# Kernel optimization log

Hardware: AMD Instinct MI355X
Metric: run time of the kernel (lower is better)

Reference implementation:

```python
import jax, jax.numpy as jnp
import numpy as np

BN_EPS = 1e-5
N_OUT, D_OUT = 64, 128


def setup_inputs() -> dict:
    key = jax.random.key(0)
    k1, k2, k3, k4 = jax.random.split(key, 4)
    B, N_in, D_in, K = 512, 64, 128, 4
    x = jax.random.normal(k1, (B, N_in, D_in), dtype=jnp.float32)
    # block-sparse weights: one (D_in x D_out) block per (output-row, active-input-row) pair
    W = jax.random.normal(k2, (N_OUT, K, D_in, D_OUT), dtype=jnp.float32) * (1.0 / np.sqrt(K * D_in))
    bias = jax.random.normal(k3, (N_OUT, D_OUT), dtype=jnp.float32) * 0.02
    gamma = jnp.ones((N_OUT * D_OUT,), dtype=jnp.float32)
    beta = jnp.zeros((N_OUT * D_OUT,), dtype=jnp.float32)
    idx = jax.random.randint(k4, (N_OUT, K), 0, N_in, dtype=jnp.int32)
    return {"x": x, "W": W, "bias": bias, "gamma": gamma, "beta": beta, "idx": idx}


def reference(x, W, bias, gamma, beta, idx):
    B = x.shape[0]
    # structured-sparse linear: gather active input rows, per-block matmul
    xg = x[:, idx, :]                                   # [B, N_out, K, D_in]
    y = jnp.einsum('bokd,okde->boe', xg, W) + bias      # [B, N_out, D_out]
    # BatchNorm1d (training-mode batch statistics) on flattened features
    yf = y.reshape(B, -1)                               # [B, N_out*D_out]
    mean = jnp.mean(yf, axis=0)
    var = jnp.mean(jnp.square(yf - mean), axis=0)       # biased variance, as in torch BN
    yn = (yf - mean) * jax.lax.rsqrt(var + BN_EPS) * gamma + beta
    # Swish: z * sigmoid(z)
    out = yn * jax.nn.sigmoid(yn)
    return out.reshape(B, N_OUT, D_OUT)
```

## Files before the change

### kernel.cpp

```cpp
#include <hip/hip_runtime.h>


typedef __attribute__((ext_vector_type(8))) __bf16 bf16x8;
typedef __attribute__((ext_vector_type(4))) float  f32x4;

#define FEAT 8192
#define LDA  40

#define PIPE_BARRIER() do { \
    __builtin_amdgcn_sched_barrier(0); \
    asm volatile("s_waitcnt lgkmcnt(0)" ::: "memory"); \
    __builtin_amdgcn_s_barrier(); \
    __builtin_amdgcn_sched_barrier(0); \
} while (0)

__global__ __launch_bounds__(1024, 4)
void fused_encoder(const float* __restrict__ x, const float* __restrict__ W,
                   const float* __restrict__ bias, const float* __restrict__ gamma,
                   const float* __restrict__ beta, const int* __restrict__ idxp,
                   float* __restrict__ out)
{
    __shared__ alignas(16) __bf16 Alds[2][512 * LDA];
    __shared__ alignas(16) __bf16 Blds[2][32 * LDA];
    __shared__ float Sred[16][32];
    __shared__ float Qred[16][32];
    __shared__ float sscale[32];
    __shared__ float sshift[32];

    const int bid = blockIdx.x;
    const int o   = ((bid >> 5) << 3) | (bid & 7);
    const int es  = (bid >> 3) & 3;
    const int e0  = es * 32;

    const int tid  = threadIdx.x;
    const int wave = tid >> 6;
    const int lane = tid & 63;
    const int lam  = lane & 15;
    const int quad = lane >> 4;

    int rsel[4];
#pragma unroll
    for (int k = 0; k < 4; ++k) rsel[k] = idxp[o * 4 + k];

    const f32x4 zero4 = {0.f, 0.f, 0.f, 0.f};
    f32x4 acc[2][2];
#pragma unroll
    for (int mi = 0; mi < 2; ++mi)
#pragma unroll
        for (int ni = 0; ni < 2; ++ni) acc[mi][ni] = zero4;

    const int m_a = tid >> 1;
    const int ca  = (tid & 1) * 16;
    const int e_b = tid & 31;
    const int d_b = tid >> 5;

    f32x4 sA0[4], sA1[4];
    float sB0, sB1;

    auto load_stage = [&](f32x4 (&SA)[4], float& SB, const int kkc) {
        const int kidx  = kkc >> 2;
        const int dbase = (kkc & 3) * 32;
        const float* xa = x + ((m_a * 64 + rsel[kidx]) * 128 + dbase + ca);
#pragma unroll
        for (int v = 0; v < 4; ++v) SA[v] = *(const f32x4*)(xa + v * 4);
        SB = W[(((o * 4 + kidx) * 128) + dbase + d_b) * 128 + e0 + e_b];
    };

    auto store_stage = [&](const f32x4 (&SA)[4], const float SB, const int buf) {
        bf16x8 p0, p1;
#pragma unroll
        for (int j = 0; j < 4; ++j) {
            p0[j]     = (__bf16)SA[0][j];
            p0[j + 4] = (__bf16)SA[1][j];
            p1[j]     = (__bf16)SA[2][j];
            p1[j + 4] = (__bf16)SA[3][j];
        }
        *(bf16x8*)&Alds[buf][m_a * LDA + ca]     = p0;
        *(bf16x8*)&Alds[buf][m_a * LDA + ca + 8] = p1;
        Blds[buf][e_b * LDA + d_b] = (__bf16)SB;
    };

    auto compute = [&](const int buf) {
        bf16x8 af[2], bfr[2];
#pragma unroll
        for (int mi = 0; mi < 2; ++mi)
            af[mi] = *(const bf16x8*)&Alds[buf][(wave * 32 + mi * 16 + lam) * LDA + quad * 8];
#pragma unroll
        for (int ni = 0; ni < 2; ++ni)
            bfr[ni] = *(const bf16x8*)&Blds[buf][(ni * 16 + lam) * LDA + quad * 8];
#pragma unroll
        for (int mi = 0; mi < 2; ++mi)
#pragma unroll
            for (int ni = 0; ni < 2; ++ni)
                acc[mi][ni] = __builtin_amdgcn_mfma_f32_16x16x32_bf16(
                    af[mi], bfr[ni], acc[mi][ni], 0, 0, 0);
    };

    load_stage(sA0, sB0, 0);
    load_stage(sA1, sB1, 1);
    store_stage(sA0, sB0, 0);
    PIPE_BARRIER();

#pragma unroll
    for (int kk = 0; kk < 16; ++kk) {
        if (kk + 2 < 16) {
            if ((kk & 1) == 0) load_stage(sA0, sB0, kk + 2);
            else               load_stage(sA1, sB1, kk + 2);
        }
        __builtin_amdgcn_sched_barrier(0);
        compute(kk & 1);
        if (kk + 1 < 16) {
            if ((kk & 1) == 0) store_stage(sA1, sB1, 1);
            else               store_stage(sA0, sB0, 0);
            PIPE_BARRIER();
        }
    }

    float bvals[2];
#pragma unroll
    for (int ni = 0; ni < 2; ++ni)
        bvals[ni] = bias[o * 128 + e0 + ni * 16 + lam];
#pragma unroll
    for (int mi = 0; mi < 2; ++mi)
#pragma unroll
        for (int ni = 0; ni < 2; ++ni)
#pragma unroll
            for (int rr = 0; rr < 4; ++rr) acc[mi][ni][rr] += bvals[ni];

#pragma unroll
    for (int ni = 0; ni < 2; ++ni) {
        float s = 0.f, q = 0.f;
#pragma unroll
        for (int mi = 0; mi < 2; ++mi)
#pragma unroll
            for (int rr = 0; rr < 4; ++rr) {
                const float v = acc[mi][ni][rr];
                s += v; q += v * v;
            }
        s += __shfl_xor(s, 16); s += __shfl_xor(s, 32);
        q += __shfl_xor(q, 16); q += __shfl_xor(q, 32);
        if (quad == 0) {
            Sred[wave][ni * 16 + lam] = s;
            Qred[wave][ni * 16 + lam] = q;
        }
    }
    __syncthreads();

    if (tid < 32) {
        float s = 0.f, q = 0.f;
#pragma unroll
        for (int w = 0; w < 16; ++w) {
            s += Sred[w][tid];
            q += Qred[w][tid];
        }
        const float mean = s * (1.0f / 512.0f);
        const float var  = q * (1.0f / 512.0f) - mean * mean;
        const float rstd = rsqrtf(var + 1e-5f);
        const float sc   = rstd * gamma[o * 128 + e0 + tid];
        sscale[tid] = sc;
        sshift[tid] = beta[o * 128 + e0 + tid] - mean * sc;
    }
    __syncthreads();

#pragma unroll
    for (int mi = 0; mi < 2; ++mi) {
        const int rowb = wave * 32 + mi * 16 + quad * 4;
#pragma unroll
        for (int ni = 0; ni < 2; ++ni) {
            const int col = ni * 16 + lam;
            const float sc = sscale[col];
            const float sh = sshift[col];
#pragma unroll
            for (int rr = 0; rr < 4; ++rr) {
                const float xn = acc[mi][ni][rr] * sc + sh;
                const float sg = 1.0f / (1.0f + __expf(-xn));
                out[(rowb + rr) * FEAT + o * 128 + e0 + col] = xn * sg;
            }
        }
    }
}

extern "C" void kernel_launch(void* const* d_in, const int* in_sizes, int n_in,
                              void* d_out, int out_size, void* d_ws, size_t ws_size,
                              hipStream_t stream)
{
    const float* x     = (const float*)d_in[0];
    const float* W     = (const float*)d_in[1];
    const float* bias  = (const float*)d_in[2];
    const float* gamma = (const float*)d_in[3];
    const float* beta  = (const float*)d_in[4];
    const int*   idx   = (const int*)d_in[5];
    float* out = (float*)d_out;

    fused_encoder<<<dim3(256), dim3(1024), 0, stream>>>(
        x, W, bias, gamma, beta, idx, out);
}
```

Baseline: 104.0 us.

## Tile blocks over batch and full output width with cooperative grid-sync BN reduction

Each block now covers 128 batch rows and all 128 output columns of one output group, instead of all 512 batch rows and 32 columns. The batch statistics are therefore split across blocks. Per-block partial sums go to workspace and are combined after a cooperative grid-wide sync. The goal is coalesced, vectorised W and x loads and less redundant x gathering per block. The cost is a grid barrier, global partial-sum traffic, and a dependence on all 256 blocks being co-resident.

```diff
diff --git a/kernel.cpp b/kernel.cpp
--- a/kernel.cpp
+++ b/kernel.cpp
@@ -1,7 +1,11 @@
 #include <hip/hip_runtime.h>
+#include <hip/hip_cooperative_groups.h>
+
+namespace cg = cooperative_groups;
 
 
 typedef __attribute__((ext_vector_type(8))) __bf16 bf16x8;
+typedef __attribute__((ext_vector_type(4))) __bf16 bf16x4;
 typedef __attribute__((ext_vector_type(4))) float  f32x4;
 
 #define FEAT 8192
@@ -15,26 +19,29 @@
 } while (0)
 
 __global__ __launch_bounds__(1024, 4)
-void fused_encoder(const float* __restrict__ x, const float* __restrict__ W,
-                   const float* __restrict__ bias, const float* __restrict__ gamma,
-                   const float* __restrict__ beta, const int* __restrict__ idxp,
-                   float* __restrict__ out)
+void fused_encoder_coop(const float* __restrict__ x, const float* __restrict__ W,
+                        const float* __restrict__ bias, const float* __restrict__ gamma,
+                        const float* __restrict__ beta, const int* __restrict__ idxp,
+                        float* __restrict__ out, float* __restrict__ psum,
+                        float* __restrict__ psq)
 {
-    __shared__ alignas(16) __bf16 Alds[2][512 * LDA];
-    __shared__ alignas(16) __bf16 Blds[2][32 * LDA];
-    __shared__ float Sred[16][32];
-    __shared__ float Qred[16][32];
-    __shared__ float sscale[32];
-    __shared__ float sshift[32];
+    __shared__ alignas(16) __bf16 Alds[2][128 * LDA];
+    __shared__ alignas(16) __bf16 Blds[2][128 * LDA];
+    __shared__ float Sred[4][128];
+    __shared__ float Qred[4][128];
+    __shared__ float sscale[128];
+    __shared__ float sshift[128];
 
     const int bid = blockIdx.x;
     const int o   = ((bid >> 5) << 3) | (bid & 7);
-    const int es  = (bid >> 3) & 3;
-    const int e0  = es * 32;
+    const int bt  = (bid >> 3) & 3;
+    const int b0  = bt * 128;
 
     const int tid  = threadIdx.x;
     const int wave = tid >> 6;
     const int lane = tid & 63;
+    const int wr   = wave >> 2;
+    const int wc   = wave & 3;
     const int lam  = lane & 15;
     const int quad = lane >> 4;
 
@@ -49,45 +56,39 @@
 #pragma unroll
         for (int ni = 0; ni < 2; ++ni) acc[mi][ni] = zero4;
 
-    const int m_a = tid >> 1;
-    const int ca  = (tid & 1) * 16;
-    const int e_b = tid & 31;
-    const int d_b = tid >> 5;
-
-    f32x4 sA0[4], sA1[4];
-    float sB0, sB1;
-
-    auto load_stage = [&](f32x4 (&SA)[4], float& SB, const int kkc) {
-        const int kidx  = kkc >> 2;
-        const int dbase = (kkc & 3) * 32;
-        const float* xa = x + ((m_a * 64 + rsel[kidx]) * 128 + dbase + ca);
-#pragma unroll
-        for (int v = 0; v < 4; ++v) SA[v] = *(const f32x4*)(xa + v * 4);
-        SB = W[(((o * 4 + kidx) * 128) + dbase + d_b) * 128 + e0 + e_b];
+    const int m_a = tid >> 3;
+    const int ca  = (tid & 7) * 4;
+    const int e_b = tid & 127;
+    const int dgb = tid >> 7;
+
+    f32x4 sA0, sA1, sB0, sB1;
+
+    auto load_stage = [&](f32x4& SA, f32x4& SB, const int kkc) {
+        const int kidx = kkc >> 2;
+        const int d0   = (kkc & 3) * 32;
+        SA = *(const f32x4*)(x + (((b0 + m_a) * 64 + rsel[kidx]) * 128 + d0 + ca));
+        const float* wp = W + (((o * 4 + kidx) * 128 + d0 + dgb * 4) * 128 + e_b);
+        f32x4 t;
+        t[0] = wp[0]; t[1] = wp[128]; t[2] = wp[256]; t[3] = wp[384];
+        SB = t;
     };
 
-    auto store_stage = [&](const f32x4 (&SA)[4], const float SB, const int buf) {
-        bf16x8 p0, p1;
-#pragma unroll
-        for (int j = 0; j < 4; ++j) {
-            p0[j]     = (__bf16)SA[0][j];
-            p0[j + 4] = (__bf16)SA[1][j];
-            p1[j]     = (__bf16)SA[2][j];
-            p1[j + 4] = (__bf16)SA[3][j];
-        }
-        *(bf16x8*)&Alds[buf][m_a * LDA + ca]     = p0;
-        *(bf16x8*)&Alds[buf][m_a * LDA + ca + 8] = p1;
-        Blds[buf][e_b * LDA + d_b] = (__bf16)SB;
+    auto store_stage = [&](const f32x4& SA, const f32x4& SB, const int buf) {
+        bf16x4 pa, pb;
+#pragma unroll
+        for (int j = 0; j < 4; ++j) { pa[j] = (__bf16)SA[j]; pb[j] = (__bf16)SB[j]; }
+        *(bf16x4*)&Alds[buf][m_a * LDA + ca]       = pa;
+        *(bf16x4*)&Blds[buf][e_b * LDA + dgb * 4]  = pb;
     };
 
     auto compute = [&](const int buf) {
         bf16x8 af[2], bfr[2];
 #pragma unroll
         for (int mi = 0; mi < 2; ++mi)
-            af[mi] = *(const bf16x8*)&Alds[buf][(wave * 32 + mi * 16 + lam) * LDA + quad * 8];
+            af[mi] = *(const bf16x8*)&Alds[buf][(wr * 32 + mi * 16 + lam) * LDA + quad * 8];
 #pragma unroll
         for (int ni = 0; ni < 2; ++ni)
-            bfr[ni] = *(const bf16x8*)&Blds[buf][(ni * 16 + lam) * LDA + quad * 8];
+            bfr[ni] = *(const bf16x8*)&Blds[buf][(wc * 32 + ni * 16 + lam) * LDA + quad * 8];
 #pragma unroll
         for (int mi = 0; mi < 2; ++mi)
 #pragma unroll
@@ -119,7 +120,7 @@
     float bvals[2];
 #pragma unroll
     for (int ni = 0; ni < 2; ++ni)
-        bvals[ni] = bias[o * 128 + e0 + ni * 16 + lam];
+        bvals[ni] = bias[o * 128 + wc * 32 + ni * 16 + lam];
 #pragma unroll
     for (int mi = 0; mi < 2; ++mi)
 #pragma unroll
@@ -140,41 +141,52 @@
         s += __shfl_xor(s, 16); s += __shfl_xor(s, 32);
         q += __shfl_xor(q, 16); q += __shfl_xor(q, 32);
         if (quad == 0) {
-            Sred[wave][ni * 16 + lam] = s;
-            Qred[wave][ni * 16 + lam] = q;
+            Sred[wr][wc * 32 + ni * 16 + lam] = s;
+            Qred[wr][wc * 32 + ni * 16 + lam] = q;
         }
     }
     __syncthreads();
 
-    if (tid < 32) {
+    if (tid < 128) {
         float s = 0.f, q = 0.f;
 #pragma unroll
-        for (int w = 0; w < 16; ++w) {
-            s += Sred[w][tid];
-            q += Qred[w][tid];
+        for (int w = 0; w < 4; ++w) { s += Sred[w][tid]; q += Qred[w][tid]; }
+        psum[(o * 4 + bt) * 128 + tid] = s;
+        psq [(o * 4 + bt) * 128 + tid] = q;
+    }
+
+    __threadfence();
+    cg::this_grid().sync();
+
+    if (tid < 128) {
+        float s = 0.f, q = 0.f;
+#pragma unroll
+        for (int t = 0; t < 4; ++t) {
+            s += psum[(o * 4 + t) * 128 + tid];
+            q += psq [(o * 4 + t) * 128 + tid];
         }
         const float mean = s * (1.0f / 512.0f);
         const float var  = q * (1.0f / 512.0f) - mean * mean;
         const float rstd = rsqrtf(var + 1e-5f);
-        const float sc   = rstd * gamma[o * 128 + e0 + tid];
+        const float sc   = rstd * gamma[o * 128 + tid];
         sscale[tid] = sc;
-        sshift[tid] = beta[o * 128 + e0 + tid] - mean * sc;
+        sshift[tid] = beta[o * 128 + tid] - mean * sc;
     }
     __syncthreads();
 
 #pragma unroll
     for (int mi = 0; mi < 2; ++mi) {
-        const int rowb = wave * 32 + mi * 16 + quad * 4;
+        const int rowb = b0 + wr * 32 + mi * 16 + quad * 4;
 #pragma unroll
         for (int ni = 0; ni < 2; ++ni) {
-            const int col = ni * 16 + lam;
+            const int col = wc * 32 + ni * 16 + lam;
             const float sc = sscale[col];
             const float sh = sshift[col];
 #pragma unroll
             for (int rr = 0; rr < 4; ++rr) {
                 const float xn = acc[mi][ni][rr] * sc + sh;
                 const float sg = 1.0f / (1.0f + __expf(-xn));
-                out[(rowb + rr) * FEAT + o * 128 + e0 + col] = xn * sg;
+                out[(rowb + rr) * FEAT + o * 128 + col] = xn * sg;
             }
         }
     }
@@ -190,8 +202,11 @@
     const float* gamma = (const float*)d_in[3];
     const float* beta  = (const float*)d_in[4];
     const int*   idx   = (const int*)d_in[5];
-    float* out = (float*)d_out;
-
-    fused_encoder<<<dim3(256), dim3(1024), 0, stream>>>(
-        x, W, bias, gamma, beta, idx, out);
+    float* out  = (float*)d_out;
+    float* psum = (float*)d_ws;
+    float* psq  = psum + 64 * 4 * 128;
+
+    void* args[] = {&x, &W, &bias, &gamma, &beta, &idx, &out, &psum, &psq};
+    hipLaunchCooperativeKernel((const void*)fused_encoder_coop,
+                               dim3(256), dim3(1024), args, 0, stream);
 }
```

New measurement: 210.0 us. 102% more time.

## Load A fragments directly from global into MFMA registers, bypassing LDS

Applied to the files above, without the earlier changes.

Each lane now reads the x rows matching its MFMA A-fragment layout straight from global memory, converts them to bf16 in registers and feeds the MFMA without staging through LDS. Only the small W tile still goes through the double-buffered LDS. This drops the large A LDS buffers, their stores and reads, and the associated LDS traffic. In exchange, global loads become less coalesced: each lane reads 32 contiguous bytes from a different row.

```diff
diff --git a/kernel.cpp b/kernel.cpp
--- a/kernel.cpp
+++ b/kernel.cpp
@@ -5,7 +5,8 @@
 typedef __attribute__((ext_vector_type(4))) float  f32x4;
 
 #define FEAT 8192
-#define LDA  40
+#define XROW 8192
+#define LDB  40
 
 #define PIPE_BARRIER() do { \
     __builtin_amdgcn_sched_barrier(0); \
@@ -20,8 +21,7 @@
                    const float* __restrict__ beta, const int* __restrict__ idxp,
                    float* __restrict__ out)
 {
-    __shared__ alignas(16) __bf16 Alds[2][512 * LDA];
-    __shared__ alignas(16) __bf16 Blds[2][32 * LDA];
+    __shared__ alignas(16) __bf16 Blds[2][32 * LDB];
     __shared__ float Sred[16][32];
     __shared__ float Qred[16][32];
     __shared__ float sscale[32];
@@ -49,45 +49,47 @@
 #pragma unroll
         for (int ni = 0; ni < 2; ++ni) acc[mi][ni] = zero4;
 
-    const int m_a = tid >> 1;
-    const int ca  = (tid & 1) * 16;
+    const float* xrow0 = x + (wave * 32 + lam)      * XROW;
+    const float* xrow1 = x + (wave * 32 + 16 + lam) * XROW;
+
     const int e_b = tid & 31;
     const int d_b = tid >> 5;
 
-    f32x4 sA0[4], sA1[4];
-    float sB0, sB1;
-
-    auto load_stage = [&](f32x4 (&SA)[4], float& SB, const int kkc) {
-        const int kidx  = kkc >> 2;
-        const int dbase = (kkc & 3) * 32;
-        const float* xa = x + ((m_a * 64 + rsel[kidx]) * 128 + dbase + ca);
-#pragma unroll
-        for (int v = 0; v < 4; ++v) SA[v] = *(const f32x4*)(xa + v * 4);
-        SB = W[(((o * 4 + kidx) * 128) + dbase + d_b) * 128 + e0 + e_b];
-    };
-
-    auto store_stage = [&](const f32x4 (&SA)[4], const float SB, const int buf) {
-        bf16x8 p0, p1;
+    f32x4 sa0[4], sa1[4];
+    float sb0, sb1;
+
+    auto loadA = [&](f32x4 (&SA)[4], const int kkc) {
+        const int r  = rsel[kkc >> 2];
+        const int dd = (kkc & 3) * 32 + quad * 8;
+        const float* p0 = xrow0 + r * 128 + dd;
+        const float* p1 = xrow1 + r * 128 + dd;
+        SA[0] = *(const f32x4*)(p0);
+        SA[1] = *(const f32x4*)(p0 + 4);
+        SA[2] = *(const f32x4*)(p1);
+        SA[3] = *(const f32x4*)(p1 + 4);
+    };
+    auto loadB = [&](float& SB, const int kkc) {
+        const int kidx = kkc >> 2;
+        const int d0   = (kkc & 3) * 32;
+        SB = W[(((o * 4 + kidx) * 128) + d0 + d_b) * 128 + e0 + e_b];
+    };
+    auto storeB = [&](const float SB, const int buf) {
+        Blds[buf][e_b * LDB + d_b] = (__bf16)SB;
+    };
+    auto cvtA = [&](const f32x4 (&SA)[4], bf16x8 (&af)[2]) {
 #pragma unroll
         for (int j = 0; j < 4; ++j) {
-            p0[j]     = (__bf16)SA[0][j];
-            p0[j + 4] = (__bf16)SA[1][j];
-            p1[j]     = (__bf16)SA[2][j];
-            p1[j + 4] = (__bf16)SA[3][j];
-        }
-        *(bf16x8*)&Alds[buf][m_a * LDA + ca]     = p0;
-        *(bf16x8*)&Alds[buf][m_a * LDA + ca + 8] = p1;
-        Blds[buf][e_b * LDA + d_b] = (__bf16)SB;
-    };
-
-    auto compute = [&](const int buf) {
-        bf16x8 af[2], bfr[2];
-#pragma unroll
-        for (int mi = 0; mi < 2; ++mi)
-            af[mi] = *(const bf16x8*)&Alds[buf][(wave * 32 + mi * 16 + lam) * LDA + quad * 8];
+            af[0][j]     = (__bf16)SA[0][j];
+            af[0][j + 4] = (__bf16)SA[1][j];
+            af[1][j]     = (__bf16)SA[2][j];
+            af[1][j + 4] = (__bf16)SA[3][j];
+        }
+    };
+    auto mma = [&](const bf16x8 (&af)[2], const int buf) {
+        bf16x8 bfr[2];
 #pragma unroll
         for (int ni = 0; ni < 2; ++ni)
-            bfr[ni] = *(const bf16x8*)&Blds[buf][(ni * 16 + lam) * LDA + quad * 8];
+            bfr[ni] = *(const bf16x8*)&Blds[buf][(ni * 16 + lam) * LDB + quad * 8];
 #pragma unroll
         for (int mi = 0; mi < 2; ++mi)
 #pragma unroll
@@ -96,22 +98,26 @@
                     af[mi], bfr[ni], acc[mi][ni], 0, 0, 0);
     };
 
-    load_stage(sA0, sB0, 0);
-    load_stage(sA1, sB1, 1);
-    store_stage(sA0, sB0, 0);
+    loadA(sa0, 0); loadB(sb0, 0);
+    loadA(sa1, 1); loadB(sb1, 1);
+    storeB(sb0, 0);
     PIPE_BARRIER();
 
 #pragma unroll
     for (int kk = 0; kk < 16; ++kk) {
-        if (kk + 2 < 16) {
-            if ((kk & 1) == 0) load_stage(sA0, sB0, kk + 2);
-            else               load_stage(sA1, sB1, kk + 2);
+        bf16x8 af[2];
+        if ((kk & 1) == 0) {
+            cvtA(sa0, af);
+            if (kk + 2 < 16) { loadA(sa0, kk + 2); loadB(sb0, kk + 2); }
+        } else {
+            cvtA(sa1, af);
+            if (kk + 2 < 16) { loadA(sa1, kk + 2); loadB(sb1, kk + 2); }
         }
         __builtin_amdgcn_sched_barrier(0);
-        compute(kk & 1);
+        mma(af, kk & 1);
         if (kk + 1 < 16) {
-            if ((kk & 1) == 0) store_stage(sA1, sB1, 1);
-            else               store_stage(sA0, sB0, 0);
+            if ((kk & 1) == 0) storeB(sb1, 1);
+            else               storeB(sb0, 0);
             PIPE_BARRIER();
         }
     }
```

After: 114.4 us. 1.1x slower.
